# Optimization experiments

Hardware: AMD Instinct MI355X
Metric: run time of the kernel (lower is better)

Reference implementation:

```python
import jax, jax.numpy as jnp
import numpy as np

N, D = 8192, 1024

def setup_inputs() -> dict:
    key = jax.random.key(0)
    ks = jax.random.split(key, 7)
    s = 1.0 / np.sqrt(D)  # mimic nn.Linear init scale
    return {
        "embeddings": jax.random.normal(ks[0], (N, D), jnp.float32),
        "Wq": jax.random.normal(ks[1], (D, D), jnp.float32) * s,
        "bq": jax.random.normal(ks[2], (D,), jnp.float32) * s,
        "Wk": jax.random.normal(ks[3], (D, D), jnp.float32) * s,
        "bk": jax.random.normal(ks[4], (D,), jnp.float32) * s,
        "Wv": jax.random.normal(ks[5], (D, D), jnp.float32) * s,
        "bv": jax.random.normal(ks[6], (D,), jnp.float32) * s,
    }

def reference(embeddings, Wq, bq, Wk, bk, Wv, bv):
    # nn.Linear: y = x @ W^T + b; weights here are stored as [out, in] equivalent (square), use x @ W.T
    q = embeddings @ Wq.T + bq          # [N, D]
    k = embeddings @ Wk.T + bk          # [N, D]
    v = embeddings @ Wv.T + bv          # [N, D]
    scores = q @ k.T                    # [N, N]  (unscaled, as in source)
    attn = jax.nn.softmax(scores, axis=-1)
    out = attn @ v                      # [N, D]
    return out[:, None, :]              # [N, 1, D] matching torch broadcasted-matmul output
```

## Files before the change

kernel.cpp:

```cpp
#include <hip/hip_runtime.h>
#include <hip/hip_fp16.h>
#include <cstdint>
#include <cstddef>

typedef _Float16 half8 __attribute__((ext_vector_type(8)));
typedef _Float16 half4 __attribute__((ext_vector_type(4)));
typedef float floatx16 __attribute__((ext_vector_type(16)));

#define N_TOK 8192
#define DIM   1024

#define EPI_F32   0
#define EPI_HILO  1
#define EPI_HI    2
#define EPI_VT    3
#define EPI_ATOM  4

__device__ __forceinline__ void async_tile16(const _Float16* gp, _Float16* lp) {
    __builtin_amdgcn_global_load_lds(
        (const __attribute__((address_space(1))) void*)gp,
        (__attribute__((address_space(3))) void*)lp, 16, 0, 0);
}

template<int BM, int BN, int BK, bool ASPLIT, int EPI, bool REMAP>
__global__ __launch_bounds__(256)
void gemm_f16(const _Float16* __restrict__ Ahi, const _Float16* __restrict__ Alo,
              const _Float16* __restrict__ B,
              int kslice, int lda, int ldb,
              void* __restrict__ C, int ldc, void* __restrict__ C2,
              const float* __restrict__ bias, const float* __restrict__ invl)
{
    constexpr int MI = BM / 64;
    constexpr int NI = BN / 64;
    constexpr int CPR = BK / 8;
    constexpr int SW  = CPR - 1;
    constexpr int RPP = 2048 / BK;
    constexpr int IA  = BM * BK / 2048;
    constexpr int IB  = BN * BK / 2048;
    constexpr int A_ELTS = BM * BK;
    constexpr int B_ELTS = BN * BK;
    __shared__ _Float16 smem[(ASPLIT ? 2 : 1) * A_ELTS + B_ELTS];
    constexpr int tAhi = 0;
    constexpr int tAlo = A_ELTS;
    constexpr int tB   = (ASPLIT ? 2 : 1) * A_ELTS;

    int bx = blockIdx.x, by = blockIdx.y, bz = blockIdx.z;
    if constexpr (REMAP) {
        const int gx = gridDim.x, gy = gridDim.y;
        const int gxy = gx * gy;
        const int nb = gxy * gridDim.z;
        const int bid = bz * gxy + by * gx + bx;
        const int nid = (bid & 7) * (nb >> 3) + (bid >> 3);
        bx = nid % gx; by = (nid / gx) % gy; bz = nid / gxy;
    }

    const int tid  = threadIdx.x;
    const int row0 = by * BM;
    const int col0 = bx * BN;
    const int lane = tid & 63;
    const int w    = tid >> 6;
    const int wm   = w & 1, wn = w >> 1;
    const int l31  = lane & 31, lhi = lane >> 5;

    floatx16 acc[MI][NI];
#pragma unroll
    for (int mi = 0; mi < MI; mi++)
#pragma unroll
        for (int ni = 0; ni < NI; ni++)
#pragma unroll
            for (int e = 0; e < 16; e++) acc[mi][ni][e] = 0.f;

    const int r_s = tid / CPR;
    const int j_s = tid % CPR;

    const int k_beg = bz * kslice;
    for (int k0 = k_beg; k0 < k_beg + kslice; k0 += BK) {
        __syncthreads();
#pragma unroll
        for (int i = 0; i < IA; i++) {
            const int r = i * RPP + r_s;
            const int jg = j_s ^ ((r >> 1) & SW);
            async_tile16(Ahi + (size_t)(row0 + r) * lda + k0 + jg * 8,
                         smem + tAhi + (i * 256 + tid) * 8);
            if constexpr (ASPLIT)
                async_tile16(Alo + (size_t)(row0 + r) * lda + k0 + jg * 8,
                             smem + tAlo + (i * 256 + tid) * 8);
        }
#pragma unroll
        for (int i = 0; i < IB; i++) {
            const int r = i * RPP + r_s;
            const int jg = j_s ^ ((r >> 1) & SW);
            async_tile16(B + (size_t)(col0 + r) * ldb + k0 + jg * 8,
                         smem + tB + (i * 256 + tid) * 8);
        }
        __syncthreads();

#pragma unroll
        for (int ks = 0; ks < BK / 16; ks++) {
            half8 af[MI], bf[NI];
            half8 al[ASPLIT ? MI : 1];
            const int cb = ks * 2 + lhi;
#pragma unroll
            for (int mi = 0; mi < MI; mi++) {
                const int r = wm * (BM / 2) + mi * 32 + l31;
                const int cj = (cb ^ ((r >> 1) & SW)) * 8;
                af[mi] = *(half8*)&smem[tAhi + r * BK + cj];
                if constexpr (ASPLIT) al[mi] = *(half8*)&smem[tAlo + r * BK + cj];
            }
#pragma unroll
            for (int ni = 0; ni < NI; ni++) {
                const int r = wn * (BN / 2) + ni * 32 + l31;
                const int cj = (cb ^ ((r >> 1) & SW)) * 8;
                bf[ni] = *(half8*)&smem[tB + r * BK + cj];
            }
#pragma unroll
            for (int mi = 0; mi < MI; mi++)
#pragma unroll
                for (int ni = 0; ni < NI; ni++) {
                    acc[mi][ni] = __builtin_amdgcn_mfma_f32_32x32x16_f16(af[mi], bf[ni], acc[mi][ni], 0, 0, 0);
                    if constexpr (ASPLIT)
                        acc[mi][ni] = __builtin_amdgcn_mfma_f32_32x32x16_f16(al[mi], bf[ni], acc[mi][ni], 0, 0, 0);
                }
        }
    }

#pragma unroll
    for (int mi = 0; mi < MI; mi++) {
#pragma unroll
        for (int ni = 0; ni < NI; ni++) {
            const int colg = col0 + wn * (BN / 2) + ni * 32 + l31;
            const int base = row0 + wm * (BM / 2) + mi * 32 + 4 * lhi;
            float bv = 0.f;
            if constexpr (EPI == EPI_HILO || EPI == EPI_HI || EPI == EPI_VT) bv = bias[colg];
#pragma unroll
            for (int g = 0; g < 4; g++) {
                const int rowb = base + 8 * g;
                if constexpr (EPI == EPI_VT) {
                    half4 hv;
#pragma unroll
                    for (int r2 = 0; r2 < 4; r2++) hv[r2] = (_Float16)(acc[mi][ni][4 * g + r2] + bv);
                    *(half4*)&((_Float16*)C)[(size_t)colg * ldc + rowb] = hv;
                } else {
#pragma unroll
                    for (int r2 = 0; r2 < 4; r2++) {
                        const int rowg = rowb + r2;
                        const float v = acc[mi][ni][4 * g + r2];
                        if constexpr (EPI == EPI_F32) {
                            ((float*)C)[(size_t)rowg * ldc + colg] = v;
                        } else if constexpr (EPI == EPI_ATOM) {
                            atomicAdd(&((float*)C)[(size_t)rowg * ldc + colg], v * invl[rowg]);
                        } else {
                            const float t = v + bv;
                            const _Float16 hi = (_Float16)t;
                            ((_Float16*)C)[(size_t)rowg * ldc + colg] = hi;
                            if constexpr (EPI == EPI_HILO)
                                ((_Float16*)C2)[(size_t)rowg * ldc + colg] = (_Float16)(t - (float)hi);
                        }
                    }
                }
            }
        }
    }
}

__global__ __launch_bounds__(256)
void zero_f32(float* __restrict__ p)
{
    const size_t i = ((size_t)blockIdx.x * 256 + threadIdx.x) * 4;
    const float4 z = {0.f, 0.f, 0.f, 0.f};
    *(float4*)(p + i) = z;
}

__global__ __launch_bounds__(256)
void split_inputs(const float* __restrict__ E,
                  const float* __restrict__ Wq, const float* __restrict__ Wk, const float* __restrict__ Wv,
                  _Float16* __restrict__ Ehi, _Float16* __restrict__ Elo,
                  _Float16* __restrict__ Wqh, _Float16* __restrict__ Wkh, _Float16* __restrict__ Wvh)
{
    const int u = blockIdx.y;
    const size_t idx = ((size_t)blockIdx.x * 256 + threadIdx.x) * 4;
    const size_t MM = (size_t)DIM * DIM;
    const float* src; _Float16* dhi; _Float16* dlo = nullptr;
    if (u < 8)      { src = E + u * MM;  dhi = Ehi + u * MM; dlo = Elo + u * MM; }
    else if (u == 8){ src = Wq; dhi = Wqh; }
    else if (u == 9){ src = Wk; dhi = Wkh; }
    else            { src = Wv; dhi = Wvh; }
    const float4 f = *(const float4*)(src + idx);
    half4 hh;
    hh[0] = (_Float16)f.x; hh[1] = (_Float16)f.y; hh[2] = (_Float16)f.z; hh[3] = (_Float16)f.w;
    *(half4*)(dhi + idx) = hh;
    if (u < 8) {
        half4 hl;
        hl[0] = (_Float16)(f.x - (float)hh[0]); hl[1] = (_Float16)(f.y - (float)hh[1]);
        hl[2] = (_Float16)(f.z - (float)hh[2]); hl[3] = (_Float16)(f.w - (float)hh[3]);
        *(half4*)(dlo + idx) = hl;
    }
}

__global__ __launch_bounds__(256)
void softmax_rows(float* __restrict__ S, float* __restrict__ inv_l)
{
    __shared__ float srow[N_TOK];
    __shared__ float red[4];
    const int tid = threadIdx.x;
    float* row = S + (size_t)blockIdx.x * N_TOK;

    float mx = -3.0e38f;
#pragma unroll
    for (int i = 0; i < 8; i++) {
        const int v = i * 256 + tid;
        const float4 f = ((const float4*)row)[v];
        ((float4*)srow)[v] = f;
        mx = fmaxf(mx, fmaxf(fmaxf(f.x, f.y), fmaxf(f.z, f.w)));
    }
#pragma unroll
    for (int off = 32; off > 0; off >>= 1) mx = fmaxf(mx, __shfl_down(mx, off));
    if ((tid & 63) == 0) red[tid >> 6] = mx;
    __syncthreads();
    mx = fmaxf(fmaxf(red[0], red[1]), fmaxf(red[2], red[3]));
    __syncthreads();

    float sum = 0.f;
    _Float16* prow = (_Float16*)row;
#pragma unroll
    for (int i = 0; i < 8; i++) {
        const int v = i * 256 + tid;
        const float4 f = ((const float4*)srow)[v];
        const float e0 = __expf(f.x - mx), e1 = __expf(f.y - mx);
        const float e2 = __expf(f.z - mx), e3 = __expf(f.w - mx);
        sum += (e0 + e1) + (e2 + e3);
        half4 h; h[0] = (_Float16)e0; h[1] = (_Float16)e1; h[2] = (_Float16)e2; h[3] = (_Float16)e3;
        ((half4*)prow)[v] = h;
    }
#pragma unroll
    for (int off = 32; off > 0; off >>= 1) sum += __shfl_down(sum, off);
    if ((tid & 63) == 0) red[tid >> 6] = sum;
    __syncthreads();
    if (tid == 0) inv_l[blockIdx.x] = 1.f / (red[0] + red[1] + red[2] + red[3]);
}

extern "C" void kernel_launch(void* const* d_in, const int* in_sizes, int n_in,
                              void* d_out, int out_size, void* d_ws, size_t ws_size,
                              hipStream_t stream)
{
    const float* E  = (const float*)d_in[0];
    const float* Wq = (const float*)d_in[1];
    const float* bq = (const float*)d_in[2];
    const float* Wk = (const float*)d_in[3];
    const float* bk = (const float*)d_in[4];
    const float* Wv = (const float*)d_in[5];
    const float* bv = (const float*)d_in[6];
    float* out = (float*)d_out;

    char* ws = (char*)d_ws;
    const size_t SZ = (size_t)N_TOK * DIM * sizeof(_Float16);
    const size_t WW = (size_t)DIM * DIM * sizeof(_Float16);
    _Float16* q_hi = (_Float16*)(ws);
    _Float16* q_lo = (_Float16*)(ws + SZ);
    _Float16* k_hi = (_Float16*)(ws + 2 * SZ);
    _Float16* vt   = (_Float16*)(ws + 3 * SZ);
    float*    invl = (float*)(ws + 4 * SZ);
    char*     scratch = ws + 4 * SZ + 65536;
    _Float16* Ehi = (_Float16*)(scratch);
    _Float16* Elo = (_Float16*)(scratch + SZ);
    _Float16* Wqh = (_Float16*)(scratch + 2 * SZ);
    _Float16* Wkh = (_Float16*)(scratch + 2 * SZ + WW);
    _Float16* Wvh = (_Float16*)(scratch + 2 * SZ + 2 * WW);
    float*    Sc  = (float*)(scratch);
    const size_t esplit_bytes = 2 * SZ + 3 * WW;
    const size_t base = 4 * SZ + 65536;

    int NC = 256;
    const int cands[6] = {8192, 4096, 2048, 1024, 512, 256};
    for (int i = 0; i < 6; i++) {
        size_t sc = (size_t)cands[i] * N_TOK * 4;
        size_t need = base + (sc > esplit_bytes ? sc : esplit_bytes);
        if (ws_size >= need) { NC = cands[i]; break; }
    }

    const dim3 blk(256, 1, 1);
    constexpr int KS = 4;

    zero_f32<<<dim3(N_TOK * DIM / 1024, 1, 1), blk, 0, stream>>>(out);

    split_inputs<<<dim3(DIM * DIM / 1024, 11, 1), blk, 0, stream>>>(
        E, Wq, Wk, Wv, Ehi, Elo, Wqh, Wkh, Wvh);

    gemm_f16<128, 64, 64, true, EPI_HILO, true><<<dim3(DIM / 64, N_TOK / 128, 1), blk, 0, stream>>>(
        Ehi, Elo, Wqh, DIM, DIM, DIM, q_hi, DIM, q_lo, bq, nullptr);
    gemm_f16<128, 64, 64, true, EPI_HI, true><<<dim3(DIM / 64, N_TOK / 128, 1), blk, 0, stream>>>(
        Ehi, Elo, Wkh, DIM, DIM, DIM, k_hi, DIM, nullptr, bk, nullptr);
    gemm_f16<128, 64, 64, false, EPI_VT, true><<<dim3(DIM / 64, N_TOK / 128, 1), blk, 0, stream>>>(
        Ehi, nullptr, Wvh, DIM, DIM, DIM, vt, N_TOK, nullptr, bv, nullptr);

    const int nchunks = N_TOK / NC;
    for (int c = 0; c < nchunks; c++) {
        const size_t roff = (size_t)c * NC;
        gemm_f16<128, 128, 64, true, EPI_F32, false><<<dim3(N_TOK / 128, NC / 128, 1), blk, 0, stream>>>(
            q_hi + roff * DIM, q_lo + roff * DIM, k_hi, DIM, DIM, DIM,
            Sc, N_TOK, nullptr, nullptr, nullptr);
        softmax_rows<<<dim3(NC, 1, 1), blk, 0, stream>>>(Sc, invl + roff);
        gemm_f16<128, 64, 64, false, EPI_ATOM, true><<<dim3(DIM / 64, NC / 128, KS), blk, 0, stream>>>(
            (const _Float16*)Sc, nullptr, vt, N_TOK / KS, 2 * N_TOK, N_TOK,
            out + roff * DIM, DIM, nullptr, nullptr, invl + roff);
    }
}
```

Before: 731.9 us.

## Fuse QKV projections into one GEMM and replace split-K atomics with partial-sum reduction

Merges the three Q/K/V projection GEMMs into a single launch with a z-dimension selecting the unit, using 128x128 tiles. It relies on Wq/Wk/Wv fp16 copies sitting contiguously in the workspace. The split-K P·V GEMM now writes fp32 partials into the unused upper half of each score row, and a small reduce kernel sums them and applies 1/l. This removes the output zeroing kernel and the atomicAdd traffic. The cost is one extra reduction pass over the partials, and the code depends on the scratch layout to avoid overwriting live fp16 probabilities.

```diff
diff --git a/kernel.cpp b/kernel.cpp
--- a/kernel.cpp
+++ b/kernel.cpp
@@ -11,10 +11,7 @@
 #define DIM   1024
 
 #define EPI_F32   0
-#define EPI_HILO  1
-#define EPI_HI    2
-#define EPI_VT    3
-#define EPI_ATOM  4
+#define EPI_PART  1
 
 __device__ __forceinline__ void async_tile16(const _Float16* gp, _Float16* lp) {
     __builtin_amdgcn_global_load_lds(
@@ -27,8 +24,7 @@
 void gemm_f16(const _Float16* __restrict__ Ahi, const _Float16* __restrict__ Alo,
               const _Float16* __restrict__ B,
               int kslice, int lda, int ldb,
-              void* __restrict__ C, int ldc, void* __restrict__ C2,
-              const float* __restrict__ bias, const float* __restrict__ invl)
+              float* __restrict__ C, int ldc)
 {
     constexpr int MI = BM / 64;
     constexpr int NI = BN / 64;
@@ -130,45 +126,165 @@
         for (int ni = 0; ni < NI; ni++) {
             const int colg = col0 + wn * (BN / 2) + ni * 32 + l31;
             const int base = row0 + wm * (BM / 2) + mi * 32 + 4 * lhi;
-            float bv = 0.f;
-            if constexpr (EPI == EPI_HILO || EPI == EPI_HI || EPI == EPI_VT) bv = bias[colg];
 #pragma unroll
             for (int g = 0; g < 4; g++) {
                 const int rowb = base + 8 * g;
-                if constexpr (EPI == EPI_VT) {
+#pragma unroll
+                for (int r2 = 0; r2 < 4; r2++) {
+                    const int rowg = rowb + r2;
+                    const float v = acc[mi][ni][4 * g + r2];
+                    if constexpr (EPI == EPI_F32) {
+                        C[(size_t)rowg * ldc + colg] = v;
+                    } else {
+                        C[(size_t)rowg * ldc + (size_t)bz * DIM + colg] = v;
+                    }
+                }
+            }
+        }
+    }
+}
+
+template<int BM, int BN, int BK>
+__global__ __launch_bounds__(256)
+void gemm_qkv(const _Float16* __restrict__ Ehi, const _Float16* __restrict__ Elo,
+              const _Float16* __restrict__ W,
+              _Float16* __restrict__ qhi, _Float16* __restrict__ qlo,
+              _Float16* __restrict__ khi, _Float16* __restrict__ vtr,
+              const float* __restrict__ bq, const float* __restrict__ bk,
+              const float* __restrict__ bv)
+{
+    constexpr int MI = BM / 64;
+    constexpr int NI = BN / 64;
+    constexpr int CPR = BK / 8;
+    constexpr int SW  = CPR - 1;
+    constexpr int RPP = 2048 / BK;
+    constexpr int IA  = BM * BK / 2048;
+    constexpr int IB  = BN * BK / 2048;
+    constexpr int A_ELTS = BM * BK;
+    constexpr int B_ELTS = BN * BK;
+    __shared__ _Float16 smem[2 * A_ELTS + B_ELTS];
+    constexpr int tAhi = 0;
+    constexpr int tAlo = A_ELTS;
+    constexpr int tB   = 2 * A_ELTS;
+
+    int bx = blockIdx.x, by = blockIdx.y, bz = blockIdx.z;
+    {
+        const int gx = gridDim.x, gy = gridDim.y;
+        const int gxy = gx * gy;
+        const int nb = gxy * gridDim.z;
+        const int bid = bz * gxy + by * gx + bx;
+        const int nid = (bid & 7) * (nb >> 3) + (bid >> 3);
+        bx = nid % gx; by = (nid / gx) % gy; bz = nid / gxy;
+    }
+    const int unit = bz;
+    const bool dolo = (unit < 2);
+
+    const int tid  = threadIdx.x;
+    const int row0 = by * BM;
+    const int col0 = bx * BN;
+    const int lane = tid & 63;
+    const int w    = tid >> 6;
+    const int wm   = w & 1, wn = w >> 1;
+    const int l31  = lane & 31, lhi = lane >> 5;
+
+    floatx16 acc[MI][NI];
+#pragma unroll
+    for (int mi = 0; mi < MI; mi++)
+#pragma unroll
+        for (int ni = 0; ni < NI; ni++)
+#pragma unroll
+            for (int e = 0; e < 16; e++) acc[mi][ni][e] = 0.f;
+
+    const int r_s = tid / CPR;
+    const int j_s = tid % CPR;
+    const size_t brow0 = (size_t)(unit * DIM + col0);
+
+    for (int k0 = 0; k0 < DIM; k0 += BK) {
+        __syncthreads();
+#pragma unroll
+        for (int i = 0; i < IA; i++) {
+            const int r = i * RPP + r_s;
+            const int jg = j_s ^ ((r >> 1) & SW);
+            async_tile16(Ehi + (size_t)(row0 + r) * DIM + k0 + jg * 8,
+                         smem + tAhi + (i * 256 + tid) * 8);
+            if (dolo)
+                async_tile16(Elo + (size_t)(row0 + r) * DIM + k0 + jg * 8,
+                             smem + tAlo + (i * 256 + tid) * 8);
+        }
+#pragma unroll
+        for (int i = 0; i < IB; i++) {
+            const int r = i * RPP + r_s;
+            const int jg = j_s ^ ((r >> 1) & SW);
+            async_tile16(W + (brow0 + r) * DIM + k0 + jg * 8,
+                         smem + tB + (i * 256 + tid) * 8);
+        }
+        __syncthreads();
+
+#pragma unroll
+        for (int ks = 0; ks < BK / 16; ks++) {
+            half8 af[MI], bf[NI], al[MI];
+            const int cb = ks * 2 + lhi;
+#pragma unroll
+            for (int mi = 0; mi < MI; mi++) {
+                const int r = wm * (BM / 2) + mi * 32 + l31;
+                const int cj = (cb ^ ((r >> 1) & SW)) * 8;
+                af[mi] = *(half8*)&smem[tAhi + r * BK + cj];
+                if (dolo) al[mi] = *(half8*)&smem[tAlo + r * BK + cj];
+            }
+#pragma unroll
+            for (int ni = 0; ni < NI; ni++) {
+                const int r = wn * (BN / 2) + ni * 32 + l31;
+                const int cj = (cb ^ ((r >> 1) & SW)) * 8;
+                bf[ni] = *(half8*)&smem[tB + r * BK + cj];
+            }
+#pragma unroll
+            for (int mi = 0; mi < MI; mi++)
+#pragma unroll
+                for (int ni = 0; ni < NI; ni++)
+                    acc[mi][ni] = __builtin_amdgcn_mfma_f32_32x32x16_f16(af[mi], bf[ni], acc[mi][ni], 0, 0, 0);
+            if (dolo) {
+#pragma unroll
+                for (int mi = 0; mi < MI; mi++)
+#pragma unroll
+                    for (int ni = 0; ni < NI; ni++)
+                        acc[mi][ni] = __builtin_amdgcn_mfma_f32_32x32x16_f16(al[mi], bf[ni], acc[mi][ni], 0, 0, 0);
+            }
+        }
+    }
+
+    const float* bias = (unit == 0) ? bq : (unit == 1) ? bk : bv;
+#pragma unroll
+    for (int mi = 0; mi < MI; mi++) {
+#pragma unroll
+        for (int ni = 0; ni < NI; ni++) {
+            const int colg = col0 + wn * (BN / 2) + ni * 32 + l31;
+            const float bb = bias[colg];
+            const int base = row0 + wm * (BM / 2) + mi * 32 + 4 * lhi;
+#pragma unroll
+            for (int g = 0; g < 4; g++) {
+                const int rowb = base + 8 * g;
+                if (unit == 2) {
                     half4 hv;
 #pragma unroll
-                    for (int r2 = 0; r2 < 4; r2++) hv[r2] = (_Float16)(acc[mi][ni][4 * g + r2] + bv);
-                    *(half4*)&((_Float16*)C)[(size_t)colg * ldc + rowb] = hv;
+                    for (int r2 = 0; r2 < 4; r2++) hv[r2] = (_Float16)(acc[mi][ni][4 * g + r2] + bb);
+                    *(half4*)&vtr[(size_t)colg * N_TOK + rowb] = hv;
                 } else {
 #pragma unroll
                     for (int r2 = 0; r2 < 4; r2++) {
                         const int rowg = rowb + r2;
-                        const float v = acc[mi][ni][4 * g + r2];
-                        if constexpr (EPI == EPI_F32) {
-                            ((float*)C)[(size_t)rowg * ldc + colg] = v;
-                        } else if constexpr (EPI == EPI_ATOM) {
-                            atomicAdd(&((float*)C)[(size_t)rowg * ldc + colg], v * invl[rowg]);
+                        const float t = acc[mi][ni][4 * g + r2] + bb;
+                        const _Float16 hi = (_Float16)t;
+                        if (unit == 0) {
+                            qhi[(size_t)rowg * DIM + colg] = hi;
+                            qlo[(size_t)rowg * DIM + colg] = (_Float16)(t - (float)hi);
                         } else {
-                            const float t = v + bv;
-                            const _Float16 hi = (_Float16)t;
-                            ((_Float16*)C)[(size_t)rowg * ldc + colg] = hi;
-                            if constexpr (EPI == EPI_HILO)
-                                ((_Float16*)C2)[(size_t)rowg * ldc + colg] = (_Float16)(t - (float)hi);
+                            khi[(size_t)rowg * DIM + colg] = hi;
                         }
                     }
                 }
             }
         }
     }
-}
-
-__global__ __launch_bounds__(256)
-void zero_f32(float* __restrict__ p)
-{
-    const size_t i = ((size_t)blockIdx.x * 256 + threadIdx.x) * 4;
-    const float4 z = {0.f, 0.f, 0.f, 0.f};
-    *(float4*)(p + i) = z;
 }
 
 __global__ __launch_bounds__(256)
@@ -239,6 +355,24 @@
     if (tid == 0) inv_l[blockIdx.x] = 1.f / (red[0] + red[1] + red[2] + red[3]);
 }
 
+__global__ __launch_bounds__(256)
+void reduce_pv(const float* __restrict__ Sc, const float* __restrict__ invl,
+               float* __restrict__ out)
+{
+    const int r  = blockIdx.x;
+    const int c4 = threadIdx.x;
+    const float* p = Sc + (size_t)r * N_TOK + N_TOK / 2 + (size_t)c4 * 4;
+    float4 s = *(const float4*)p;
+#pragma unroll
+    for (int z = 1; z < 4; z++) {
+        const float4 t = *(const float4*)(p + (size_t)z * DIM);
+        s.x += t.x; s.y += t.y; s.z += t.z; s.w += t.w;
+    }
+    const float iv = invl[r];
+    float4 o; o.x = s.x * iv; o.y = s.y * iv; o.z = s.z * iv; o.w = s.w * iv;
+    *(float4*)(out + (size_t)r * DIM + (size_t)c4 * 4) = o;
+}
+
 extern "C" void kernel_launch(void* const* d_in, const int* in_sizes, int n_in,
                               void* d_out, int out_size, void* d_ws, size_t ws_size,
                               hipStream_t stream)
@@ -281,27 +415,21 @@
     const dim3 blk(256, 1, 1);
     constexpr int KS = 4;
 
-    zero_f32<<<dim3(N_TOK * DIM / 1024, 1, 1), blk, 0, stream>>>(out);
-
     split_inputs<<<dim3(DIM * DIM / 1024, 11, 1), blk, 0, stream>>>(
         E, Wq, Wk, Wv, Ehi, Elo, Wqh, Wkh, Wvh);
 
-    gemm_f16<128, 64, 64, true, EPI_HILO, true><<<dim3(DIM / 64, N_TOK / 128, 1), blk, 0, stream>>>(
-        Ehi, Elo, Wqh, DIM, DIM, DIM, q_hi, DIM, q_lo, bq, nullptr);
-    gemm_f16<128, 64, 64, true, EPI_HI, true><<<dim3(DIM / 64, N_TOK / 128, 1), blk, 0, stream>>>(
-        Ehi, Elo, Wkh, DIM, DIM, DIM, k_hi, DIM, nullptr, bk, nullptr);
-    gemm_f16<128, 64, 64, false, EPI_VT, true><<<dim3(DIM / 64, N_TOK / 128, 1), blk, 0, stream>>>(
-        Ehi, nullptr, Wvh, DIM, DIM, DIM, vt, N_TOK, nullptr, bv, nullptr);
+    gemm_qkv<128, 128, 64><<<dim3(DIM / 128, N_TOK / 128, 3), blk, 0, stream>>>(
+        Ehi, Elo, Wqh, q_hi, q_lo, k_hi, vt, bq, bk, bv);
 
     const int nchunks = N_TOK / NC;
     for (int c = 0; c < nchunks; c++) {
         const size_t roff = (size_t)c * NC;
         gemm_f16<128, 128, 64, true, EPI_F32, false><<<dim3(N_TOK / 128, NC / 128, 1), blk, 0, stream>>>(
-            q_hi + roff * DIM, q_lo + roff * DIM, k_hi, DIM, DIM, DIM,
-            Sc, N_TOK, nullptr, nullptr, nullptr);
+            q_hi + roff * DIM, q_lo + roff * DIM, k_hi, DIM, DIM, DIM, Sc, N_TOK);
         softmax_rows<<<dim3(NC, 1, 1), blk, 0, stream>>>(Sc, invl + roff);
-        gemm_f16<128, 64, 64, false, EPI_ATOM, true><<<dim3(DIM / 64, NC / 128, KS), blk, 0, stream>>>(
+        gemm_f16<128, 128, 64, false, EPI_PART, true><<<dim3(DIM / 128, NC / 128, KS), blk, 0, stream>>>(
             (const _Float16*)Sc, nullptr, vt, N_TOK / KS, 2 * N_TOK, N_TOK,
-            out + roff * DIM, DIM, nullptr, nullptr, invl + roff);
-    }
-}
+            Sc + N_TOK / 2, N_TOK);
+        reduce_pv<<<dim3(NC, 1, 1), blk, 0, stream>>>(Sc, invl + roff, out + roff * DIM);
+    }
+}
```

New measurement: 721.2 us. About the same (-1.5%).
